# Kernel tuning notes

Measured on AMD Instinct MI355X. Metric: run time of the kernel, lower is better.

Reference implementation:

```python
import jax, jax.numpy as jnp
import numpy as np

EMBED_DIM = 512
NUM_HEADS = 8
N_WIRES = 8  # kernel uses only first N_WIRES dims of each head vector


def setup_inputs() -> dict:
    key = jax.random.key(0)
    x = jax.random.normal(key, (8, 1024, EMBED_DIM), dtype=jnp.float32)
    return {"x": x}


def reference(x):
    B, S, E = x.shape
    H = NUM_HEADS
    dk = E // H
    # [B, H, S, dk]
    xh = x.reshape(B, S, H, dk).transpose(0, 2, 1, 3)
    # Quantum RY-overlap kernel closed form:
    #   RY(-y) RY(x) |0> = RY(x - y) |0>  =>  <0...0|psi> = prod_w cos((x_w - y_w)/2)
    # Only the first N_WIRES components of each head vector are used
    # (states.view(-1)[0] reads the first batch row's |0..0> amplitude).
    xw = xh[..., :N_WIRES]  # [B, H, S, NW]
    scores = jnp.ones((B, H, S, S), dtype=x.dtype)
    for w in range(N_WIRES):  # fixed small loop, fuses under jit
        diff = xw[:, :, :, None, w] - xw[:, :, None, :, w]  # [B, H, S, S]
        scores = scores * jnp.cos(diff * 0.5)
    scores = jnp.abs(scores)
    attn = jax.nn.softmax(scores, axis=-1)  # dropout is identity at eval
    out = jnp.einsum("bhij,bhjd->bhid", attn, xh)  # [B, H, S, dk]
    return out.transpose(0, 2, 1, 3).reshape(B, S, E)
```

## Files before the change

### kernel.cpp

```cpp
#include <hip/hip_runtime.h>

#define B_  8
#define S_  1024
#define E_  512
#define TI  128
#define TJ  32
#define P_STR 40

typedef _Float16 half_t;
typedef _Float16 half4_t __attribute__((ext_vector_type(4)));
typedef _Float16 half8_t __attribute__((ext_vector_type(8)));
typedef float    floatx16 __attribute__((ext_vector_type(16)));

__global__ __launch_bounds__(256) void phi_kernel(const float* __restrict__ x,
                                                  half_t* __restrict__ phi) {
    int idx = blockIdx.x * 256 + threadIdx.x;
    int bh = idx >> 10, j = idx & 1023;
    int b = bh >> 3, h = bh & 7;
    const float* px = x + ((size_t)(b * S_ + j)) * E_ + h * 64;
    float4 w0 = ((const float4*)px)[0];
    float4 w1 = ((const float4*)px)[1];
    float xi[8] = {w0.x, w0.y, w0.z, w0.w, w1.x, w1.y, w1.z, w1.w};
    float c[8], s[8];
    #pragma unroll
    for (int w = 0; w < 8; ++w) {
        float v = xi[w] * 0.5f;
        c[w] = __cosf(v);
        s[w] = __sinf(v);
    }
    float p01[4] = {c[0]*c[1], s[0]*c[1], c[0]*s[1], s[0]*s[1]};
    float p23[4] = {c[2]*c[3], s[2]*c[3], c[2]*s[3], s[2]*s[3]};
    float p45[4] = {c[4]*c[5], s[4]*c[5], c[4]*s[5], s[4]*s[5]};
    float p67[4] = {c[6]*c[7], s[6]*c[7], c[6]*s[7], s[6]*s[7]};
    half_t o[32];
    #pragma unroll
    for (int kk = 0; kk < 16; ++kk) {
        o[kk]      = (half_t)(p01[kk & 3] * p23[kk >> 2]);
        o[16 + kk] = (half_t)(p45[kk & 3] * p67[kk >> 2]);
    }
    half8_t* dst = (half8_t*)(phi + (size_t)idx * 32);
    dst[0] = *(half8_t*)&o[0];
    dst[1] = *(half8_t*)&o[8];
    dst[2] = *(half8_t*)&o[16];
    dst[3] = *(half8_t*)&o[24];
}

__global__ __launch_bounds__(256) void vt_kernel(const float* __restrict__ x,
                                                 half_t* __restrict__ vt) {
    int bh = blockIdx.x >> 5, j0 = (blockIdx.x & 31) * 32;
    int b = bh >> 3, h = bh & 7;
    int t = threadIdx.x;
    __shared__ half_t sh[64 * P_STR];
    int jj = t >> 3, lo = t & 7, d0 = lo * 8;
    const float* src = x + ((size_t)(b * S_ + j0 + jj)) * E_ + h * 64 + d0;
    float4 a = ((const float4*)src)[0];
    float4 cc = ((const float4*)src)[1];
    float vals[8] = {a.x, a.y, a.z, a.w, cc.x, cc.y, cc.z, cc.w};
    #pragma unroll
    for (int nq = 0; nq < 8; ++nq) {
        int q = (nq + lo) & 7;
        sh[(d0 + q) * P_STR + jj] = (half_t)vals[q];
    }
    __syncthreads();
    int d = t >> 2, seg = t & 3;
    half8_t v = *(half8_t*)&sh[d * P_STR + seg * 8];
    *(half8_t*)(vt + ((size_t)(bh * 64 + d)) * 1024 + j0 + seg * 8) = v;
}

__global__ __launch_bounds__(256, 2) void attn_phi_kernel(const half_t* __restrict__ phi,
                                                          const half_t* __restrict__ vt,
                                                          float* __restrict__ out) {
    const int bh = blockIdx.x;
    const int b  = bh >> 3, h = bh & 7;
    const int i0 = blockIdx.y * TI;
    const int t  = threadIdx.x;
    const int wv = t >> 6;
    const int ln = t & 63;
    const int m  = ln & 31;
    const int hf = ln >> 5;

    __shared__ __align__(16) half_t sh_p[TI * P_STR];
    __shared__ float sh_den[TI];

    const half_t* phibh = phi + (size_t)bh * (1024 * 32);
    const half_t* vtbh  = vt  + (size_t)bh * (64 * 1024);

    const half_t* pi = phibh + (size_t)(i0 + wv * 32 + m) * 32 + hf * 8;
    half8_t biL = *(const half8_t*)pi;
    half8_t biH = *(const half8_t*)(pi + 16);

    floatx16 acc0, acc1, z;
    #pragma unroll
    for (int k = 0; k < 16; ++k) { acc0[k] = 0.f; acc1[k] = 0.f; z[k] = 0.f; }
    float dacc0 = 0.f, dacc1 = 0.f;

    const int irow = wv * 32 + m;
    const half_t* prow = &sh_p[irow * P_STR];

    const half_t* pj  = phibh + (size_t)m * 32 + hf * 8;
    const half_t* v0p = vtbh + (size_t)m * 1024 + hf * 8;
    const half_t* v1p = vtbh + (size_t)(32 + m) * 1024 + hf * 8;
    half8_t ajL = *(const half8_t*)pj;
    half8_t ajH = *(const half8_t*)(pj + 16);
    half8_t b00 = *(const half8_t*)v0p;
    half8_t b01 = *(const half8_t*)(v0p + 16);
    half8_t b10 = *(const half8_t*)v1p;
    half8_t b11 = *(const half8_t*)(v1p + 16);

    for (int j0 = 0; j0 < S_; j0 += TJ) {
        int jn = (j0 + TJ) & (S_ - 1);
        const half_t* pjn  = phibh + (size_t)(jn + m) * 32 + hf * 8;
        const half_t* v0pn = vtbh + (size_t)m * 1024 + jn + hf * 8;
        const half_t* v1pn = vtbh + (size_t)(32 + m) * 1024 + jn + hf * 8;
        half8_t najL = *(const half8_t*)pjn;
        half8_t najH = *(const half8_t*)(pjn + 16);
        half8_t nb00 = *(const half8_t*)v0pn;
        half8_t nb01 = *(const half8_t*)(v0pn + 16);
        half8_t nb10 = *(const half8_t*)v1pn;
        half8_t nb11 = *(const half8_t*)(v1pn + 16);

        floatx16 sH = __builtin_amdgcn_mfma_f32_32x32x16_f16(ajH, biH, z, 0, 0, 0);
        floatx16 sL = __builtin_amdgcn_mfma_f32_32x32x16_f16(ajL, biL, z, 0, 0, 0);

        #pragma unroll
        for (int g = 0; g < 4; ++g) {
            half4_t pk;
            #pragma unroll
            for (int r = 0; r < 4; ++r) {
                float sc = sH[4 * g + r] * sL[4 * g + r];
                float p = __expf(__builtin_fabsf(sc));
                if (r & 1) dacc1 += p; else dacc0 += p;
                pk[r] = (half_t)p;
            }
            *(half4_t*)&sh_p[irow * P_STR + g * 8 + hf * 4] = pk;
        }

        half8_t ap0 = *(const half8_t*)(prow + hf * 8);
        half8_t ap1 = *(const half8_t*)(prow + 16 + hf * 8);
        acc0 = __builtin_amdgcn_mfma_f32_32x32x16_f16(ap0, b00, acc0, 0, 0, 0);
        acc0 = __builtin_amdgcn_mfma_f32_32x32x16_f16(ap1, b01, acc0, 0, 0, 0);
        acc1 = __builtin_amdgcn_mfma_f32_32x32x16_f16(ap0, b10, acc1, 0, 0, 0);
        acc1 = __builtin_amdgcn_mfma_f32_32x32x16_f16(ap1, b11, acc1, 0, 0, 0);

        ajL = najL; ajH = najH;
        b00 = nb00; b01 = nb01; b10 = nb10; b11 = nb11;
    }

    float dacc = dacc0 + dacc1;
    dacc += __shfl_xor(dacc, 32, 64);
    sh_den[wv * 32 + m] = dacc;
    __syncthreads();

    #pragma unroll
    for (int reg = 0; reg < 16; ++reg) {
        int il = (reg & 3) + 8 * (reg >> 2) + 4 * hf;
        float inv = 1.f / sh_den[wv * 32 + il];
        size_t base = ((size_t)(b * S_ + i0 + wv * 32 + il)) * E_ + h * 64 + m;
        out[base]      = acc0[reg] * inv;
        out[base + 32] = acc1[reg] * inv;
    }
}

__device__ __forceinline__ void make_frags_fb(float4 w0, float4 w1, int hf,
                                              half8_t* fH, half8_t* fL) {
    float xi[8] = {w0.x, w0.y, w0.z, w0.w, w1.x, w1.y, w1.z, w1.w};
    float c[8], s[8];
    #pragma unroll
    for (int w = 0; w < 8; ++w) {
        float v = xi[w] * 0.5f;
        c[w] = __cosf(v);
        s[w] = __sinf(v);
    }
    float p01[4] = {c[0]*c[1], s[0]*c[1], c[0]*s[1], s[0]*s[1]};
    float p23[4] = {c[2]*c[3], s[2]*c[3], c[2]*s[3], s[2]*s[3]};
    float p45[4] = {c[4]*c[5], s[4]*c[5], c[4]*s[5], s[4]*s[5]};
    float p67[4] = {c[6]*c[7], s[6]*c[7], c[6]*s[7], s[6]*s[7]};
    #pragma unroll
    for (int idx = 0; idx < 8; ++idx) {
        int a = idx & 3;
        int bsel = (idx >> 2) | (hf << 1);
        (*fL)[idx] = (half_t)(p01[a] * p23[bsel]);
        (*fH)[idx] = (half_t)(p45[a] * p67[bsel]);
    }
}

__global__ __launch_bounds__(256, 2) void attn_fb_kernel(const float* __restrict__ x,
                                                         float* __restrict__ out) {
    const int bh = blockIdx.x;
    const int b  = bh >> 3, h = bh & 7;
    const int i0 = blockIdx.y * TI;
    const int t  = threadIdx.x;
    const int wv = t >> 6, ln = t & 63, m = ln & 31, hf = ln >> 5, lo = t & 7;
    __shared__ __align__(16) half_t sh_p[TI * P_STR];
    __shared__ __align__(16) half_t sh_v[64 * P_STR];
    __shared__ float sh_den[TI];
    const float* xh = x + (size_t)b * S_ * E_ + h * 64;
    half8_t biH, biL;
    {
        const float* px = xh + (size_t)(i0 + wv * 32 + m) * E_;
        make_frags_fb(((const float4*)px)[0], ((const float4*)px)[1], hf, &biH, &biL);
    }
    floatx16 acc0, acc1, z;
    #pragma unroll
    for (int k = 0; k < 16; ++k) { acc0[k] = 0.f; acc1[k] = 0.f; z[k] = 0.f; }
    float dacc = 0.f;
    const int sv_j = t >> 3, sv_d0 = lo * 8;
    for (int j0 = 0; j0 < S_; j0 += TJ) {
        __syncthreads();
        const float* pjx = xh + (size_t)(j0 + m) * E_;
        float4 jw0 = ((const float4*)pjx)[0];
        float4 jw1 = ((const float4*)pjx)[1];
        const float* pv = xh + (size_t)(j0 + sv_j) * E_ + sv_d0;
        float4 v0 = ((const float4*)pv)[0];
        float4 v1 = ((const float4*)pv)[1];
        half8_t ajH, ajL;
        make_frags_fb(jw0, jw1, hf, &ajH, &ajL);
        {
            float vals[8] = {v0.x, v0.y, v0.z, v0.w, v1.x, v1.y, v1.z, v1.w};
            #pragma unroll
            for (int nq = 0; nq < 8; ++nq) {
                int q = (nq + lo) & 7;
                sh_v[(sv_d0 + q) * P_STR + sv_j] = (half_t)vals[q];
            }
        }
        __syncthreads();
        floatx16 sH = __builtin_amdgcn_mfma_f32_32x32x16_f16(ajH, biH, z, 0, 0, 0);
        floatx16 sL = __builtin_amdgcn_mfma_f32_32x32x16_f16(ajL, biL, z, 0, 0, 0);
        const int irow = wv * 32 + m;
        #pragma unroll
        for (int g = 0; g < 4; ++g) {
            half4_t pk;
            #pragma unroll
            for (int r = 0; r < 4; ++r) {
                float sc = sH[4 * g + r] * sL[4 * g + r];
                float p = __expf(__builtin_fabsf(sc));
                dacc += p;
                pk[r] = (half_t)p;
            }
            *(half4_t*)&sh_p[irow * P_STR + g * 8 + hf * 4] = pk;
        }
        const half_t* prow = &sh_p[(wv * 32 + m) * P_STR];
        half8_t ap0 = *(const half8_t*)(prow + hf * 8);
        half8_t ap1 = *(const half8_t*)(prow + 16 + hf * 8);
        const half_t* vr0 = &sh_v[m * P_STR];
        const half_t* vr1 = &sh_v[(32 + m) * P_STR];
        half8_t b00 = *(const half8_t*)(vr0 + hf * 8);
        half8_t b01 = *(const half8_t*)(vr0 + 16 + hf * 8);
        half8_t b10 = *(const half8_t*)(vr1 + hf * 8);
        half8_t b11 = *(const half8_t*)(vr1 + 16 + hf * 8);
        acc0 = __builtin_amdgcn_mfma_f32_32x32x16_f16(ap0, b00, acc0, 0, 0, 0);
        acc0 = __builtin_amdgcn_mfma_f32_32x32x16_f16(ap1, b01, acc0, 0, 0, 0);
        acc1 = __builtin_amdgcn_mfma_f32_32x32x16_f16(ap0, b10, acc1, 0, 0, 0);
        acc1 = __builtin_amdgcn_mfma_f32_32x32x16_f16(ap1, b11, acc1, 0, 0, 0);
    }
    dacc += __shfl_xor(dacc, 32, 64);
    sh_den[wv * 32 + m] = dacc;
    __syncthreads();
    #pragma unroll
    for (int reg = 0; reg < 16; ++reg) {
        int il = (reg & 3) + 8 * (reg >> 2) + 4 * hf;
        float inv = 1.f / sh_den[wv * 32 + il];
        size_t base = ((size_t)(b * S_ + i0 + wv * 32 + il)) * E_ + h * 64 + m;
        out[base]      = acc0[reg] * inv;
        out[base + 32] = acc1[reg] * inv;
    }
}

extern "C" void kernel_launch(void* const* d_in, const int* in_sizes, int n_in,
                              void* d_out, int out_size, void* d_ws, size_t ws_size,
                              hipStream_t stream) {
    const float* x = (const float*)d_in[0];
    float* out = (float*)d_out;
    const size_t PHI_BYTES = (size_t)64 * 1024 * 32 * sizeof(half_t);
    const size_t VT_BYTES  = (size_t)64 * 64 * 1024 * sizeof(half_t);
    if (ws_size >= PHI_BYTES + VT_BYTES) {
        half_t* phi = (half_t*)d_ws;
        half_t* vt  = (half_t*)((char*)d_ws + PHI_BYTES);
        phi_kernel<<<dim3(64 * 1024 / 256), 256, 0, stream>>>(x, phi);
        vt_kernel<<<dim3(64 * 32), 256, 0, stream>>>(x, vt);
        attn_phi_kernel<<<dim3(B_ * 8, S_ / TI), 256, 0, stream>>>(phi, vt, out);
    } else {
        attn_fb_kernel<<<dim3(B_ * 8, S_ / TI), 256, 0, stream>>>(x, out);
    }
}
```

Measured before the change: 112.3 us.

## Split key dimension across waves with LDS reduction and merge prep kernels

```diff
diff --git a/kernel.cpp b/kernel.cpp
--- a/kernel.cpp
+++ b/kernel.cpp
@@ -3,8 +3,6 @@
 #define B_  8
 #define S_  1024
 #define E_  512
-#define TI  128
-#define TJ  32
 #define P_STR 40
 
 typedef _Float16 half_t;
@@ -12,80 +10,95 @@
 typedef _Float16 half8_t __attribute__((ext_vector_type(8)));
 typedef float    floatx16 __attribute__((ext_vector_type(16)));
 
-__global__ __launch_bounds__(256) void phi_kernel(const float* __restrict__ x,
-                                                  half_t* __restrict__ phi) {
-    int idx = blockIdx.x * 256 + threadIdx.x;
-    int bh = idx >> 10, j = idx & 1023;
-    int b = bh >> 3, h = bh & 7;
-    const float* px = x + ((size_t)(b * S_ + j)) * E_ + h * 64;
-    float4 w0 = ((const float4*)px)[0];
-    float4 w1 = ((const float4*)px)[1];
-    float xi[8] = {w0.x, w0.y, w0.z, w0.w, w1.x, w1.y, w1.z, w1.w};
-    float c[8], s[8];
-    #pragma unroll
-    for (int w = 0; w < 8; ++w) {
-        float v = xi[w] * 0.5f;
-        c[w] = __cosf(v);
-        s[w] = __sinf(v);
-    }
-    float p01[4] = {c[0]*c[1], s[0]*c[1], c[0]*s[1], s[0]*s[1]};
-    float p23[4] = {c[2]*c[3], s[2]*c[3], c[2]*s[3], s[2]*s[3]};
-    float p45[4] = {c[4]*c[5], s[4]*c[5], c[4]*s[5], s[4]*s[5]};
-    float p67[4] = {c[6]*c[7], s[6]*c[7], c[6]*s[7], s[6]*s[7]};
-    half_t o[32];
-    #pragma unroll
-    for (int kk = 0; kk < 16; ++kk) {
-        o[kk]      = (half_t)(p01[kk & 3] * p23[kk >> 2]);
-        o[16 + kk] = (half_t)(p45[kk & 3] * p67[kk >> 2]);
-    }
-    half8_t* dst = (half8_t*)(phi + (size_t)idx * 32);
-    dst[0] = *(half8_t*)&o[0];
-    dst[1] = *(half8_t*)&o[8];
-    dst[2] = *(half8_t*)&o[16];
-    dst[3] = *(half8_t*)&o[24];
-}
-
-__global__ __launch_bounds__(256) void vt_kernel(const float* __restrict__ x,
-                                                 half_t* __restrict__ vt) {
-    int bh = blockIdx.x >> 5, j0 = (blockIdx.x & 31) * 32;
-    int b = bh >> 3, h = bh & 7;
-    int t = threadIdx.x;
-    __shared__ half_t sh[64 * P_STR];
-    int jj = t >> 3, lo = t & 7, d0 = lo * 8;
-    const float* src = x + ((size_t)(b * S_ + j0 + jj)) * E_ + h * 64 + d0;
-    float4 a = ((const float4*)src)[0];
-    float4 cc = ((const float4*)src)[1];
-    float vals[8] = {a.x, a.y, a.z, a.w, cc.x, cc.y, cc.z, cc.w};
-    #pragma unroll
-    for (int nq = 0; nq < 8; ++nq) {
-        int q = (nq + lo) & 7;
-        sh[(d0 + q) * P_STR + jj] = (half_t)vals[q];
-    }
-    __syncthreads();
-    int d = t >> 2, seg = t & 3;
-    half8_t v = *(half8_t*)&sh[d * P_STR + seg * 8];
-    *(half8_t*)(vt + ((size_t)(bh * 64 + d)) * 1024 + j0 + seg * 8) = v;
-}
-
-__global__ __launch_bounds__(256, 2) void attn_phi_kernel(const half_t* __restrict__ phi,
-                                                          const half_t* __restrict__ vt,
-                                                          float* __restrict__ out) {
+__device__ __forceinline__ void st4(float* dst, const floatx16& a, int q) {
+    float4 v;
+    v.x = a[q * 4 + 0]; v.y = a[q * 4 + 1];
+    v.z = a[q * 4 + 2]; v.w = a[q * 4 + 3];
+    *(float4*)dst = v;
+}
+__device__ __forceinline__ void add4(floatx16& a, int q, const float* src) {
+    float4 v = *(const float4*)src;
+    a[q * 4 + 0] += v.x; a[q * 4 + 1] += v.y;
+    a[q * 4 + 2] += v.z; a[q * 4 + 3] += v.w;
+}
+
+__global__ __launch_bounds__(256) void pre_kernel(const float* __restrict__ x,
+                                                  half_t* __restrict__ phi,
+                                                  half_t* __restrict__ vt) {
+    if (blockIdx.x < 256) {
+        int idx = blockIdx.x * 256 + threadIdx.x;
+        int bh = idx >> 10, j = idx & 1023;
+        int b = bh >> 3, h = bh & 7;
+        const float* px = x + ((size_t)(b * S_ + j)) * E_ + h * 64;
+        float4 w0 = ((const float4*)px)[0];
+        float4 w1 = ((const float4*)px)[1];
+        float xi[8] = {w0.x, w0.y, w0.z, w0.w, w1.x, w1.y, w1.z, w1.w};
+        float c[8], s[8];
+        #pragma unroll
+        for (int w = 0; w < 8; ++w) {
+            float v = xi[w] * 0.5f;
+            c[w] = __cosf(v);
+            s[w] = __sinf(v);
+        }
+        float p01[4] = {c[0]*c[1], s[0]*c[1], c[0]*s[1], s[0]*s[1]};
+        float p23[4] = {c[2]*c[3], s[2]*c[3], c[2]*s[3], s[2]*s[3]};
+        float p45[4] = {c[4]*c[5], s[4]*c[5], c[4]*s[5], s[4]*s[5]};
+        float p67[4] = {c[6]*c[7], s[6]*c[7], c[6]*s[7], s[6]*s[7]};
+        half_t o[32];
+        #pragma unroll
+        for (int kk = 0; kk < 16; ++kk) {
+            o[kk]      = (half_t)(p01[kk & 3] * p23[kk >> 2]);
+            o[16 + kk] = (half_t)(p45[kk & 3] * p67[kk >> 2]);
+        }
+        half8_t* dst = (half8_t*)(phi + (size_t)idx * 32);
+        dst[0] = *(half8_t*)&o[0];
+        dst[1] = *(half8_t*)&o[8];
+        dst[2] = *(half8_t*)&o[16];
+        dst[3] = *(half8_t*)&o[24];
+    } else {
+        int blk = blockIdx.x - 256;
+        int bh = blk >> 5, j0 = (blk & 31) * 32;
+        int b = bh >> 3, h = bh & 7;
+        int t = threadIdx.x;
+        __shared__ half_t sh[64 * P_STR];
+        int jj = t >> 3, lo = t & 7, d0 = lo * 8;
+        const float* src = x + ((size_t)(b * S_ + j0 + jj)) * E_ + h * 64 + d0;
+        float4 a = ((const float4*)src)[0];
+        float4 cc = ((const float4*)src)[1];
+        float vals[8] = {a.x, a.y, a.z, a.w, cc.x, cc.y, cc.z, cc.w};
+        #pragma unroll
+        for (int nq = 0; nq < 8; ++nq) {
+            int q = (nq + lo) & 7;
+            sh[(d0 + q) * P_STR + jj] = (half_t)vals[q];
+        }
+        __syncthreads();
+        int d = t >> 2, seg = t & 3;
+        half8_t v = *(half8_t*)&sh[d * P_STR + seg * 8];
+        *(half8_t*)(vt + ((size_t)(bh * 64 + d)) * 1024 + j0 + seg * 8) = v;
+    }
+}
+
+__global__ __launch_bounds__(256, 8) void attn_kernel(const half_t* __restrict__ phi,
+                                                      const half_t* __restrict__ vt,
+                                                      float* __restrict__ out) {
     const int bh = blockIdx.x;
     const int b  = bh >> 3, h = bh & 7;
-    const int i0 = blockIdx.y * TI;
+    const int i0 = blockIdx.y * 32;
     const int t  = threadIdx.x;
     const int wv = t >> 6;
     const int ln = t & 63;
     const int m  = ln & 31;
     const int hf = ln >> 5;
 
-    __shared__ __align__(16) half_t sh_p[TI * P_STR];
-    __shared__ float sh_den[TI];
+    __shared__ __align__(16) char raw[4 * 32 * P_STR * 2];
+    half_t* sh_p   = (half_t*)raw;
+    float*  sh_red = (float*)raw;
+    __shared__ float sh_den[128];
 
     const half_t* phibh = phi + (size_t)bh * (1024 * 32);
     const half_t* vtbh  = vt  + (size_t)bh * (64 * 1024);
 
-    const half_t* pi = phibh + (size_t)(i0 + wv * 32 + m) * 32 + hf * 8;
+    const half_t* pi = phibh + (size_t)(i0 + m) * 32 + hf * 8;
     half8_t biL = *(const half8_t*)pi;
     half8_t biH = *(const half8_t*)(pi + 16);
 
@@ -94,12 +107,12 @@
     for (int k = 0; k < 16; ++k) { acc0[k] = 0.f; acc1[k] = 0.f; z[k] = 0.f; }
     float dacc0 = 0.f, dacc1 = 0.f;
 
-    const int irow = wv * 32 + m;
-    const half_t* prow = &sh_p[irow * P_STR];
-
-    const half_t* pj  = phibh + (size_t)m * 32 + hf * 8;
-    const half_t* v0p = vtbh + (size_t)m * 1024 + hf * 8;
-    const half_t* v1p = vtbh + (size_t)(32 + m) * 1024 + hf * 8;
+    half_t* prow = sh_p + (wv * 32 + m) * P_STR;
+    const int jbase = wv * 256;
+
+    const half_t* pj  = phibh + (size_t)(jbase + m) * 32 + hf * 8;
+    const half_t* v0p = vtbh + (size_t)m * 1024 + jbase + hf * 8;
+    const half_t* v1p = vtbh + (size_t)(32 + m) * 1024 + jbase + hf * 8;
     half8_t ajL = *(const half8_t*)pj;
     half8_t ajH = *(const half8_t*)(pj + 16);
     half8_t b00 = *(const half8_t*)v0p;
@@ -107,8 +120,8 @@
     half8_t b10 = *(const half8_t*)v1p;
     half8_t b11 = *(const half8_t*)(v1p + 16);
 
-    for (int j0 = 0; j0 < S_; j0 += TJ) {
-        int jn = (j0 + TJ) & (S_ - 1);
+    for (int k = 0; k < 8; ++k) {
+        int jn = (jbase + k * 32 + 32) & (S_ - 1);
         const half_t* pjn  = phibh + (size_t)(jn + m) * 32 + hf * 8;
         const half_t* v0pn = vtbh + (size_t)m * 1024 + jn + hf * 8;
         const half_t* v1pn = vtbh + (size_t)(32 + m) * 1024 + jn + hf * 8;
@@ -132,7 +145,7 @@
                 if (r & 1) dacc1 += p; else dacc0 += p;
                 pk[r] = (half_t)p;
             }
-            *(half4_t*)&sh_p[irow * P_STR + g * 8 + hf * 4] = pk;
+            *(half4_t*)&prow[g * 8 + hf * 4] = pk;
         }
 
         half8_t ap0 = *(const half8_t*)(prow + hf * 8);
@@ -149,120 +162,51 @@
     float dacc = dacc0 + dacc1;
     dacc += __shfl_xor(dacc, 32, 64);
     sh_den[wv * 32 + m] = dacc;
-    __syncthreads();
-
-    #pragma unroll
-    for (int reg = 0; reg < 16; ++reg) {
-        int il = (reg & 3) + 8 * (reg >> 2) + 4 * hf;
-        float inv = 1.f / sh_den[wv * 32 + il];
-        size_t base = ((size_t)(b * S_ + i0 + wv * 32 + il)) * E_ + h * 64 + m;
-        out[base]      = acc0[reg] * inv;
-        out[base + 32] = acc1[reg] * inv;
-    }
-}
-
-__device__ __forceinline__ void make_frags_fb(float4 w0, float4 w1, int hf,
-                                              half8_t* fH, half8_t* fL) {
-    float xi[8] = {w0.x, w0.y, w0.z, w0.w, w1.x, w1.y, w1.z, w1.w};
-    float c[8], s[8];
-    #pragma unroll
-    for (int w = 0; w < 8; ++w) {
-        float v = xi[w] * 0.5f;
-        c[w] = __cosf(v);
-        s[w] = __sinf(v);
-    }
-    float p01[4] = {c[0]*c[1], s[0]*c[1], c[0]*s[1], s[0]*s[1]};
-    float p23[4] = {c[2]*c[3], s[2]*c[3], c[2]*s[3], s[2]*s[3]};
-    float p45[4] = {c[4]*c[5], s[4]*c[5], c[4]*s[5], s[4]*s[5]};
-    float p67[4] = {c[6]*c[7], s[6]*c[7], c[6]*s[7], s[6]*s[7]};
-    #pragma unroll
-    for (int idx = 0; idx < 8; ++idx) {
-        int a = idx & 3;
-        int bsel = (idx >> 2) | (hf << 1);
-        (*fL)[idx] = (half_t)(p01[a] * p23[bsel]);
-        (*fH)[idx] = (half_t)(p45[a] * p67[bsel]);
-    }
-}
-
-__global__ __launch_bounds__(256, 2) void attn_fb_kernel(const float* __restrict__ x,
-                                                         float* __restrict__ out) {
-    const int bh = blockIdx.x;
-    const int b  = bh >> 3, h = bh & 7;
-    const int i0 = blockIdx.y * TI;
-    const int t  = threadIdx.x;
-    const int wv = t >> 6, ln = t & 63, m = ln & 31, hf = ln >> 5, lo = t & 7;
-    __shared__ __align__(16) half_t sh_p[TI * P_STR];
-    __shared__ __align__(16) half_t sh_v[64 * P_STR];
-    __shared__ float sh_den[TI];
-    const float* xh = x + (size_t)b * S_ * E_ + h * 64;
-    half8_t biH, biL;
-    {
-        const float* px = xh + (size_t)(i0 + wv * 32 + m) * E_;
-        make_frags_fb(((const float4*)px)[0], ((const float4*)px)[1], hf, &biH, &biL);
-    }
-    floatx16 acc0, acc1, z;
-    #pragma unroll
-    for (int k = 0; k < 16; ++k) { acc0[k] = 0.f; acc1[k] = 0.f; z[k] = 0.f; }
-    float dacc = 0.f;
-    const int sv_j = t >> 3, sv_d0 = lo * 8;
-    for (int j0 = 0; j0 < S_; j0 += TJ) {
-        __syncthreads();
-        const float* pjx = xh + (size_t)(j0 + m) * E_;
-        float4 jw0 = ((const float4*)pjx)[0];
-        float4 jw1 = ((const float4*)pjx)[1];
-        const float* pv = xh + (size_t)(j0 + sv_j) * E_ + sv_d0;
-        float4 v0 = ((const float4*)pv)[0];
-        float4 v1 = ((const float4*)pv)[1];
-        half8_t ajH, ajL;
-        make_frags_fb(jw0, jw1, hf, &ajH, &ajL);
-        {
-            float vals[8] = {v0.x, v0.y, v0.z, v0.w, v1.x, v1.y, v1.z, v1.w};
-            #pragma unroll
-            for (int nq = 0; nq < 8; ++nq) {
-                int q = (nq + lo) & 7;
-                sh_v[(sv_d0 + q) * P_STR + sv_j] = (half_t)vals[q];
-            }
-        }
-        __syncthreads();
-        floatx16 sH = __builtin_amdgcn_mfma_f32_32x32x16_f16(ajH, biH, z, 0, 0, 0);
-        floatx16 sL = __builtin_amdgcn_mfma_f32_32x32x16_f16(ajL, biL, z, 0, 0, 0);
-        const int irow = wv * 32 + m;
-        #pragma unroll
-        for (int g = 0; g < 4; ++g) {
-            half4_t pk;
-            #pragma unroll
-            for (int r = 0; r < 4; ++r) {
-                float sc = sH[4 * g + r] * sL[4 * g + r];
-                float p = __expf(__builtin_fabsf(sc));
-                dacc += p;
-                pk[r] = (half_t)p;
-            }
-            *(half4_t*)&sh_p[irow * P_STR + g * 8 + hf * 4] = pk;
-        }
-        const half_t* prow = &sh_p[(wv * 32 + m) * P_STR];
-        half8_t ap0 = *(const half8_t*)(prow + hf * 8);
-        half8_t ap1 = *(const half8_t*)(prow + 16 + hf * 8);
-        const half_t* vr0 = &sh_v[m * P_STR];
-        const half_t* vr1 = &sh_v[(32 + m) * P_STR];
-        half8_t b00 = *(const half8_t*)(vr0 + hf * 8);
-        half8_t b01 = *(const half8_t*)(vr0 + 16 + hf * 8);
-        half8_t b10 = *(const half8_t*)(vr1 + hf * 8);
-        half8_t b11 = *(const half8_t*)(vr1 + 16 + hf * 8);
-        acc0 = __builtin_amdgcn_mfma_f32_32x32x16_f16(ap0, b00, acc0, 0, 0, 0);
-        acc0 = __builtin_amdgcn_mfma_f32_32x32x16_f16(ap1, b01, acc0, 0, 0, 0);
-        acc1 = __builtin_amdgcn_mfma_f32_32x32x16_f16(ap0, b10, acc1, 0, 0, 0);
-        acc1 = __builtin_amdgcn_mfma_f32_32x32x16_f16(ap1, b11, acc1, 0, 0, 0);
-    }
-    dacc += __shfl_xor(dacc, 32, 64);
-    sh_den[wv * 32 + m] = dacc;
-    __syncthreads();
-    #pragma unroll
-    for (int reg = 0; reg < 16; ++reg) {
-        int il = (reg & 3) + 8 * (reg >> 2) + 4 * hf;
-        float inv = 1.f / sh_den[wv * 32 + il];
-        size_t base = ((size_t)(b * S_ + i0 + wv * 32 + il)) * E_ + h * 64 + m;
-        out[base]      = acc0[reg] * inv;
-        out[base + 32] = acc1[reg] * inv;
+
+    __syncthreads();
+    if (wv == 3) {
+        #pragma unroll
+        for (int q = 0; q < 4; ++q) {
+            st4(&sh_red[q * 256 + ln * 4], acc0, q);
+            st4(&sh_red[(4 + q) * 256 + ln * 4], acc1, q);
+        }
+    }
+    __syncthreads();
+    if (wv == 2) {
+        #pragma unroll
+        for (int q = 0; q < 4; ++q) {
+            add4(acc0, q, &sh_red[q * 256 + ln * 4]);
+            add4(acc1, q, &sh_red[(4 + q) * 256 + ln * 4]);
+            st4(&sh_red[q * 256 + ln * 4], acc0, q);
+            st4(&sh_red[(4 + q) * 256 + ln * 4], acc1, q);
+        }
+    }
+    __syncthreads();
+    if (wv == 1) {
+        #pragma unroll
+        for (int q = 0; q < 4; ++q) {
+            add4(acc0, q, &sh_red[q * 256 + ln * 4]);
+            add4(acc1, q, &sh_red[(4 + q) * 256 + ln * 4]);
+            st4(&sh_red[q * 256 + ln * 4], acc0, q);
+            st4(&sh_red[(4 + q) * 256 + ln * 4], acc1, q);
+        }
+    }
+    __syncthreads();
+    if (wv == 0) {
+        #pragma unroll
+        for (int q = 0; q < 4; ++q) {
+            add4(acc0, q, &sh_red[q * 256 + ln * 4]);
+            add4(acc1, q, &sh_red[(4 + q) * 256 + ln * 4]);
+        }
+        #pragma unroll
+        for (int reg = 0; reg < 16; ++reg) {
+            int il = (reg & 3) + 8 * (reg >> 2) + 4 * hf;
+            float den = sh_den[il] + sh_den[32 + il] + sh_den[64 + il] + sh_den[96 + il];
+            float inv = 1.f / den;
+            size_t base = ((size_t)(b * S_ + i0 + il)) * E_ + h * 64 + m;
+            out[base]      = acc0[reg] * inv;
+            out[base + 32] = acc1[reg] * inv;
+        }
     }
 }
 
@@ -272,14 +216,8 @@
     const float* x = (const float*)d_in[0];
     float* out = (float*)d_out;
     const size_t PHI_BYTES = (size_t)64 * 1024 * 32 * sizeof(half_t);
-    const size_t VT_BYTES  = (size_t)64 * 64 * 1024 * sizeof(half_t);
-    if (ws_size >= PHI_BYTES + VT_BYTES) {
-        half_t* phi = (half_t*)d_ws;
-        half_t* vt  = (half_t*)((char*)d_ws + PHI_BYTES);
-        phi_kernel<<<dim3(64 * 1024 / 256), 256, 0, stream>>>(x, phi);
-        vt_kernel<<<dim3(64 * 32), 256, 0, stream>>>(x, vt);
-        attn_phi_kernel<<<dim3(B_ * 8, S_ / TI), 256, 0, stream>>>(phi, vt, out);
-    } else {
-        attn_fb_kernel<<<dim3(B_ * 8, S_ / TI), 256, 0, stream>>>(x, out);
-    }
-}
+    half_t* phi = (half_t*)d_ws;
+    half_t* vt  = (half_t*)((char*)d_ws + PHI_BYTES);
+    pre_kernel<<<dim3(256 + 2048), 256, 0, stream>>>(x, phi, vt);
+    attn_kernel<<<dim3(64, 32), 256, 0, stream>>>(phi, vt, out);
+}
```

Measured after the change: 267.9 us. 2.39x slower.
